# Kernel tuning notes

Hardware: AMD Instinct MI355X
Metric: run time of the kernel (lower is better)

Reference implementation:

```python
import jax, jax.numpy as jnp
import numpy as np

THETA_BASE = 10000.0

def rope(x, pos_offset=0):
    # x: (B, S, D), D even. Rotates interleaved (even, odd) dim pairs.
    B, S, D = x.shape
    pos = jnp.arange(pos_offset, pos_offset + S, dtype=jnp.float32)[:, None]  # (S,1)
    p = jnp.arange(D // 2, dtype=jnp.float32)  # p-1 in source, 0-indexed here
    theta = pos * (THETA_BASE ** (-2.0 * p / D))  # (S, D//2)
    sin_t, cos_t = jnp.sin(theta), jnp.cos(theta)
    x1, x2 = x[..., 0::2], x[..., 1::2]
    r1 = x1 * cos_t - x2 * sin_t
    r2 = x1 * sin_t + x2 * cos_t
    return jnp.stack((r1, r2), axis=-1).reshape(B, S, D)

def setup_inputs() -> dict:
    key = jax.random.key(0)
    k1, k2, k3, k4 = jax.random.split(key, 4)
    B, S, E, Dh = 4, 4096, 2048, 128
    return {
        "x": jax.random.normal(k1, (B, S, E), dtype=jnp.float32),
        "W_Q": jax.random.normal(k2, (E, Dh), dtype=jnp.float32) / np.sqrt(E),
        "W_K": jax.random.normal(k3, (E, Dh), dtype=jnp.float32) / np.sqrt(E),
        "W_V": jax.random.normal(k4, (E, Dh), dtype=jnp.float32) / np.sqrt(E),
    }

def reference(x, W_Q, W_K, W_V):
    d_h = W_Q.shape[1]
    past_len = 0  # kv_cache is None (prefill)
    Q = rope(x @ W_Q, pos_offset=past_len)  # NOTE: source ropes Q and V, not K
    K = x @ W_K
    V = rope(x @ W_V, pos_offset=past_len)
    scores = jnp.einsum('bqd,bkd->bqk', Q, K) / jnp.sqrt(jnp.float32(d_h))
    S_q, S_total = scores.shape[-2], scores.shape[-1]
    i = jnp.arange(S_q)[:, None] + past_len
    j = jnp.arange(S_total)[None, :]
    causal = j <= i  # (S_q, S_total) bool
    masked = jnp.where(causal[None, :, :], scores, jnp.float32(-jnp.inf))
    attn = jax.nn.softmax(masked, axis=-1)
    return jnp.einsum('bqk,bkd->bqd', attn, V)
```

## Files before the change

### kernel.cpp

```cpp
#include <hip/hip_runtime.h>
#include <hip/hip_bf16.h>
#include <stdint.h>

#define S_LEN 4096
#define E_DIM 2048
#define DH    128

typedef __bf16 bf16_t;
typedef bf16_t bf16x8 __attribute__((ext_vector_type(8)));
typedef float  f32x4  __attribute__((ext_vector_type(4)));

__device__ __forceinline__ unsigned short f2bf(float f) {
  union { float f; uint32_t u; } v; v.f = f;
  uint32_t u = v.u;
  uint32_t r = (u + 0x7fffu + ((u >> 16) & 1u)) >> 16;
  return (unsigned short)r;
}

__device__ __forceinline__ bf16x8 ld_bf16x8(const unsigned short* p) {
  return *(const bf16x8*)p;
}

__device__ __forceinline__ f32x4 mfma16(bf16x8 a, bf16x8 b, f32x4 c) {
  return __builtin_amdgcn_mfma_f32_16x16x32_bf16(a, b, c, 0, 0, 0);
}

__device__ __forceinline__ void gload16(const void* gsrc, void* ldst) {
  __builtin_amdgcn_global_load_lds(
      (const __attribute__((address_space(1))) uint32_t*)gsrc,
      (__attribute__((address_space(3))) uint32_t*)ldst, 16, 0, 0);
}

__global__ __launch_bounds__(256) void prep_kernel(
    const float* __restrict__ WQ, const float* __restrict__ WK,
    const float* __restrict__ WV,
    float2* __restrict__ trig, unsigned short* __restrict__ Wt)
{
  const int bx  = blockIdx.x;
  const int tid = threadIdx.x;
  if (bx < 1024) {
    const int idx = bx * 256 + tid;
    const int pos = idx >> 6, p = idx & 63;
    const float freq = powf(10000.0f, -(float)p / 64.0f);
    float sv, cv;
    sincosf((float)pos * freq, &sv, &cv);
    trig[idx] = make_float2(cv, sv);
    return;
  }
  __shared__ float lds[64][65];
  const int t   = bx - 1024;
  const int z   = t >> 6;
  const int rem = t & 63;
  const int k0  = (rem >> 1) * 64;
  const int n0  = (rem & 1) * 64;
  const float* W = (z == 0) ? WQ : ((z == 1) ? WK : WV);
  #pragma unroll
  for (int pass = 0; pass < 4; pass++) {
    const int r  = pass * 16 + (tid >> 4);
    const int c4 = (tid & 15) * 4;
    float4 v = *(const float4*)(W + (size_t)(k0 + r) * 128 + n0 + c4);
    lds[c4 + 0][r] = v.x; lds[c4 + 1][r] = v.y;
    lds[c4 + 2][r] = v.z; lds[c4 + 3][r] = v.w;
  }
  __syncthreads();
  #pragma unroll
  for (int pass = 0; pass < 4; pass++) {
    const int n  = pass * 16 + (tid >> 4);
    const int k4 = (tid & 15) * 4;
    ushort4 pk;
    pk.x = f2bf(lds[n][k4 + 0]); pk.y = f2bf(lds[n][k4 + 1]);
    pk.z = f2bf(lds[n][k4 + 2]); pk.w = f2bf(lds[n][k4 + 3]);
    *(ushort4*)(Wt + (size_t)(z * 128 + n0 + n) * E_DIM + k0 + k4) = pk;
  }
}

__global__ __launch_bounds__(256, 2) void proj_kernel(
    const float* __restrict__ x, const unsigned short* __restrict__ Wt,
    const float2* __restrict__ trig,
    unsigned short* __restrict__ Qb, unsigned short* __restrict__ Kb,
    unsigned short* __restrict__ Vt)
{
  __shared__ __align__(16) uint8_t Abuf[2][128 * 128];
  __shared__ __align__(16) uint8_t Bbuf[2][96 * 128];

  const int tid  = threadIdx.x;
  const int lane = tid & 63, w2 = tid >> 6;
  const int wr = w2 & 1, wc = w2 >> 1;
  const int col = lane & 15, kg = lane >> 4;

  const int m0 = blockIdx.x * 128;
  const int p  = blockIdx.y;

  f32x4 acc[4][3];
  #pragma unroll
  for (int i = 0; i < 4; i++)
    #pragma unroll
    for (int j = 0; j < 3; j++) acc[i][j] = (f32x4){0.f, 0.f, 0.f, 0.f};

  const int a_r = lane >> 4;
  const int a_c = (lane & 15) * 4;
  const int b_r  = lane >> 3;
  const int b_cb = (lane & 7) * 16;

  float4 a_reg[8];

  #define ALOAD(K0)                                                           \
    do {                                                                      \
      _Pragma("unroll")                                                       \
      for (int j = 0; j < 8; j++) {                                           \
        const int row = w2 * 32 + j * 4 + a_r;                                \
        a_reg[j] = *(const float4*)(x + (size_t)(m0 + row) * E_DIM + (K0) + a_c);\
      }                                                                       \
    } while (0)

  #define BSTAGE(K0, BUF)                                                     \
    do {                                                                      \
      _Pragma("unroll")                                                       \
      for (int c = 0; c < 3; c++) {                                           \
        const int seg = w2 * 3 + c;                                           \
        const int row = seg * 8 + b_r;                                        \
        const int src = b_cb ^ ((row & 7) << 4);                              \
        gload16((const char*)Wt + ((size_t)(p * 96 + row) * E_DIM + (K0)) * 2 + src,\
                &Bbuf[BUF][seg * 1024]);                                      \
      }                                                                       \
    } while (0)

  #define AWRITE(BUF)                                                         \
    do {                                                                      \
      _Pragma("unroll")                                                       \
      for (int j = 0; j < 8; j++) {                                           \
        const int row = w2 * 32 + j * 4 + a_r;                                \
        ushort4 h;                                                            \
        h.x = f2bf(a_reg[j].x); h.y = f2bf(a_reg[j].y);                       \
        h.z = f2bf(a_reg[j].z); h.w = f2bf(a_reg[j].w);                       \
        const int dst = (a_c * 2) ^ ((row & 7) << 4);                         \
        *(ushort4*)(&Abuf[BUF][row * 128 + dst]) = h;                         \
      }                                                                       \
    } while (0)

  ALOAD(0);
  BSTAGE(0, 0);
  AWRITE(0);
  __syncthreads();

  int cur = 0;
  for (int t = 0; t < 32; t++) {
    if (t < 31) {
      ALOAD((t + 1) * 64);
      BSTAGE((t + 1) * 64, cur ^ 1);
    }

    __builtin_amdgcn_s_setprio(1);
    #pragma unroll
    for (int kk = 0; kk < 2; kk++) {
      bf16x8 af[4];
      #pragma unroll
      for (int i = 0; i < 4; i++) {
        const int row = wr * 64 + i * 16 + col;
        af[i] = *(const bf16x8*)(&Abuf[cur][row * 128 +
                 ((kk * 64 + kg * 16) ^ ((row & 7) << 4))]);
      }
      #pragma unroll
      for (int ns = 0; ns < 3; ns++) {
        const int n = wc * 48 + ns * 16 + col;
        bf16x8 bf = *(const bf16x8*)(&Bbuf[cur][n * 128 +
                    ((kk * 64 + kg * 16) ^ ((n & 7) << 4))]);
        #pragma unroll
        for (int i = 0; i < 4; i++)
          acc[i][ns] = mfma16(af[i], bf, acc[i][ns]);
      }
    }
    __builtin_amdgcn_s_setprio(0);

    if (t < 31) AWRITE(cur ^ 1);
    __syncthreads();
    cur ^= 1;
  }
  #undef ALOAD
  #undef BSTAGE
  #undef AWRITE

  #pragma unroll
  for (int i = 0; i < 4; i++) {
    const int mbase = m0 + wr * 64 + i * 16 + kg * 4;
    const int spos  = mbase & 4095;
    const int bb    = mbase >> 12;
    #pragma unroll
    for (int ns = 0; ns < 3; ns++) {
      const int n = p * 96 + wc * 48 + ns * 16 + col;
      const int z = n >> 7, d = n & 127;
      f32x4 v = acc[i][ns];
      if (z == 1) {
        #pragma unroll
        for (int r = 0; r < 4; r++)
          Kb[(size_t)(mbase + r) * DH + d] = f2bf(v[r]);
      } else {
        const float sgn  = (d & 1) ? 1.0f : -1.0f;
        const int   pidx = d >> 1;
        float ov[4];
        #pragma unroll
        for (int r = 0; r < 4; r++) {
          float  pv = __shfl_xor(v[r], 1, 64);
          float2 cs = trig[(spos + r) * 64 + pidx];
          ov[r] = v[r] * cs.x + sgn * pv * cs.y;
        }
        if (z == 0) {
          #pragma unroll
          for (int r = 0; r < 4; r++)
            Qb[(size_t)(mbase + r) * DH + d] =
                f2bf(ov[r] * 0.08838834764831845f);
        } else {
          ushort4 pk;
          pk.x = f2bf(ov[0]); pk.y = f2bf(ov[1]);
          pk.z = f2bf(ov[2]); pk.w = f2bf(ov[3]);
          *(ushort4*)(Vt + ((size_t)(bb * DH + d)) * S_LEN + spos) = pk;
        }
      }
    }
  }
}

__global__ __launch_bounds__(256, 2) void flash_kernel(
    const unsigned short* __restrict__ Qb, const unsigned short* __restrict__ Kb,
    const unsigned short* __restrict__ Vt, float* __restrict__ out)
{
  __shared__ __align__(16) unsigned short Ktile[128 * 128];
  __shared__ __align__(16) unsigned short Vtile[128 * 128];
  __shared__ __align__(16) unsigned short Plds[4][16][72];

  const int bid  = blockIdx.x;
  const int half = bid >> 8, rb = bid & 255;
  const int qi   = half ? (127 - (rb >> 1)) : (rb >> 1);
  const int b    = (rb & 1) | (half << 1);
  const int q0   = qi * 32;

  const int tid = threadIdx.x;
  const int lane = tid & 63, w = tid >> 6;
  const int h   = w & 1;
  const int kvh = w >> 1;
  const int col = lane & 15, kg = lane >> 4;

  bf16x8 qf[4];
  {
    const unsigned short* qrow =
        Qb + (size_t)(b * S_LEN + q0 + h * 16 + col) * DH;
    #pragma unroll
    for (int kk = 0; kk < 4; kk++)
      qf[kk] = ld_bf16x8(qrow + kk * 32 + kg * 8);
  }

  f32x4 o[8];
  #pragma unroll
  for (int i = 0; i < 8; i++) o[i] = (f32x4){0.f, 0.f, 0.f, 0.f};
  float mrow[4] = {-1e30f, -1e30f, -1e30f, -1e30f};
  float lrow[4] = {0.f, 0.f, 0.f, 0.f};

  const char* Kbase = (const char*)(Kb + (size_t)b * S_LEN * DH);
  const char* Vbase = (const char*)(Vt + (size_t)b * DH * S_LEN);

  const int r_off = lane >> 4, colb = (lane & 15) * 16;

  for (int kv0 = 0; kv0 < q0 + 32; kv0 += 128) {
    #pragma unroll
    for (int c = 0; c < 8; c++) {
      const int row = w * 32 + c * 4 + r_off;
      const int src = colb ^ ((row & 7) << 4);
      gload16(Kbase + (size_t)(kv0 + row) * 256 + src,
              (char*)Ktile + w * 8192 + c * 1024);
    }
    #pragma unroll
    for (int c = 0; c < 8; c++) {
      const int d   = w * 32 + c * 4 + r_off;
      const int src = colb ^ ((d & 7) << 4);
      gload16(Vbase + (size_t)d * 8192 + (size_t)kv0 * 2 + src,
              (char*)Vtile + w * 8192 + c * 1024);
    }
    __syncthreads();

    f32x4 st[4];
    __builtin_amdgcn_s_setprio(1);
    #pragma unroll
    for (int kb = 0; kb < 4; kb++) {
      f32x4 sacc = (f32x4){0.f, 0.f, 0.f, 0.f};
      const int krow = kvh * 64 + kb * 16 + col;
      #pragma unroll
      for (int kk = 0; kk < 4; kk++) {
        bf16x8 kf = *(const bf16x8*)((const char*)Ktile + krow * 256 +
                                     ((kk * 64 + kg * 16) ^ ((krow & 7) << 4)));
        sacc = mfma16(qf[kk], kf, sacc);
      }
      st[kb] = sacc;
    }
    __builtin_amdgcn_s_setprio(0);

    if (kv0 + 127 > q0) {
      #pragma unroll
      for (int kb = 0; kb < 4; kb++) {
        const int key = kv0 + kvh * 64 + kb * 16 + col;
        #pragma unroll
        for (int r = 0; r < 4; r++) {
          const int q = q0 + h * 16 + kg * 4 + r;
          if (key > q) st[kb][r] = -1e30f;
        }
      }
    }

    float scale[4];
    #pragma unroll
    for (int r = 0; r < 4; r++) {
      float mx = fmaxf(fmaxf(st[0][r], st[1][r]), fmaxf(st[2][r], st[3][r]));
      #pragma unroll
      for (int off = 1; off < 16; off <<= 1)
        mx = fmaxf(mx, __shfl_xor(mx, off, 64));
      const float mnew = fmaxf(mrow[r], mx);
      scale[r] = __expf(mrow[r] - mnew);
      mrow[r] = mnew;
      float psum = 0.f;
      #pragma unroll
      for (int kb = 0; kb < 4; kb++) {
        float pexp = __expf(st[kb][r] - mnew);
        st[kb][r] = pexp;
        psum += pexp;
      }
      lrow[r] = lrow[r] * scale[r] + psum;
    }
    #pragma unroll
    for (int nt = 0; nt < 8; nt++)
      #pragma unroll
      for (int r = 0; r < 4; r++)
        o[nt][r] *= scale[r];

    #pragma unroll
    for (int kb = 0; kb < 4; kb++)
      #pragma unroll
      for (int r = 0; r < 4; r++)
        Plds[w][kg * 4 + r][kb * 16 + col] = f2bf(st[kb][r]);

    __builtin_amdgcn_s_setprio(1);
    #pragma unroll
    for (int kc = 0; kc < 2; kc++) {
      bf16x8 pa = ld_bf16x8(&Plds[w][col][kc * 32 + kg * 8]);
      #pragma unroll
      for (int nt = 0; nt < 8; nt++) {
        const int vrow = nt * 16 + col;
        bf16x8 vf = *(const bf16x8*)((const char*)Vtile + vrow * 256 +
            ((kvh * 128 + kc * 64 + kg * 16) ^ ((vrow & 7) << 4)));
        o[nt] = mfma16(pa, vf, o[nt]);
      }
    }
    __builtin_amdgcn_s_setprio(0);
    __syncthreads();
  }

  float lfull[4];
  #pragma unroll
  for (int r = 0; r < 4; r++) {
    float l = lrow[r];
    #pragma unroll
    for (int off = 1; off < 16; off <<= 1)
      l += __shfl_xor(l, off, 64);
    lfull[r] = l;
  }

  float* Olds = (float*)Ktile;
  float* Ml   = (float*)Vtile;
  #pragma unroll
  for (int nt = 0; nt < 8; nt++)
    #pragma unroll
    for (int r = 0; r < 4; r++)
      Olds[(w * 16 + kg * 4 + r) * 128 + nt * 16 + col] = o[nt][r];
  if (col == 0) {
    #pragma unroll
    for (int r = 0; r < 4; r++) {
      Ml[w * 16 + kg * 4 + r]      = mrow[r];
      Ml[64 + w * 16 + kg * 4 + r] = lfull[r];
    }
  }
  __syncthreads();
  if (w < 2) {
    #pragma unroll
    for (int r = 0; r < 4; r++) {
      const int row = kg * 4 + r;
      const float m1 = Ml[w * 16 + row],        l1 = Ml[64 + w * 16 + row];
      const float m2 = Ml[(w + 2) * 16 + row],  l2 = Ml[64 + (w + 2) * 16 + row];
      const float mf = fmaxf(m1, m2);
      const float w1 = __expf(m1 - mf), wgt2 = __expf(m2 - mf);
      const float inv = 1.0f / (l1 * w1 + l2 * wgt2);
      float* orow = out + (size_t)(b * S_LEN + q0 + w * 16 + row) * DH;
      #pragma unroll
      for (int nt = 0; nt < 8; nt++) {
        const float v1 = Olds[(w * 16 + row) * 128 + nt * 16 + col];
        const float v2 = Olds[((w + 2) * 16 + row) * 128 + nt * 16 + col];
        orow[nt * 16 + col] = (v1 * w1 + v2 * wgt2) * inv;
      }
    }
  }
}

extern "C" void kernel_launch(void* const* d_in, const int* in_sizes, int n_in,
                              void* d_out, int out_size, void* d_ws, size_t ws_size,
                              hipStream_t stream) {
  const float* x  = (const float*)d_in[0];
  const float* WQ = (const float*)d_in[1];
  const float* WK = (const float*)d_in[2];
  const float* WV = (const float*)d_in[3];
  float* out = (float*)d_out;

  char* ws = (char*)d_ws;
  float2*         trig = (float2*)(ws);
  unsigned short* Wt   = (unsigned short*)(ws + (2u << 20));
  unsigned short* Qb   = (unsigned short*)(ws + (4u << 20));
  unsigned short* Kb   = (unsigned short*)(ws + (8u << 20));
  unsigned short* Vt   = (unsigned short*)(ws + (12u << 20));

  hipLaunchKernelGGL(prep_kernel, dim3(1216), dim3(256), 0, stream,
                     WQ, WK, WV, trig, Wt);
  hipLaunchKernelGGL(proj_kernel, dim3(128, 4), dim3(256), 0, stream,
                     x, Wt, trig, Qb, Kb, Vt);
  hipLaunchKernelGGL(flash_kernel, dim3(512), dim3(256), 0, stream,
                     Qb, Kb, Vt, out);
}
```

Baseline: 136.1 us.

## Shrink flash blocks to 16 queries and load V fragments directly from global

The flash kernel now uses 128-thread blocks, each covering 16 query rows, with two waves splitting each 128-key tile, and the grid doubles to 1024 blocks. V is no longer staged in LDS; each wave loads its V fragments straight from global memory into registers. The goal is to cut LDS footprint and improve occupancy and load balance. In exchange, reuse of K/V per block drops, total global and L2 traffic roughly doubles, and the direct V loads are uncoalesced strided reads with high register pressure.

Measured after the change: 154.2 us. 1.13x slower.

```diff
diff --git a/kernel.cpp b/kernel.cpp
--- a/kernel.cpp
+++ b/kernel.cpp
@@ -220,30 +220,26 @@
   }
 }
 
-__global__ __launch_bounds__(256, 2) void flash_kernel(
+__global__ __launch_bounds__(128, 2) void flash_kernel(
     const unsigned short* __restrict__ Qb, const unsigned short* __restrict__ Kb,
     const unsigned short* __restrict__ Vt, float* __restrict__ out)
 {
   __shared__ __align__(16) unsigned short Ktile[128 * 128];
-  __shared__ __align__(16) unsigned short Vtile[128 * 128];
-  __shared__ __align__(16) unsigned short Plds[4][16][72];
+  __shared__ __align__(16) unsigned short Plds[2][16][72];
 
   const int bid  = blockIdx.x;
-  const int half = bid >> 8, rb = bid & 255;
-  const int qi   = half ? (127 - (rb >> 1)) : (rb >> 1);
+  const int half = bid >> 9, rb = bid & 511;
+  const int qi   = half ? (255 - (rb >> 1)) : (rb >> 1);
   const int b    = (rb & 1) | (half << 1);
-  const int q0   = qi * 32;
+  const int q0   = qi * 16;
 
   const int tid = threadIdx.x;
   const int lane = tid & 63, w = tid >> 6;
-  const int h   = w & 1;
-  const int kvh = w >> 1;
   const int col = lane & 15, kg = lane >> 4;
 
   bf16x8 qf[4];
   {
-    const unsigned short* qrow =
-        Qb + (size_t)(b * S_LEN + q0 + h * 16 + col) * DH;
+    const unsigned short* qrow = Qb + (size_t)(b * S_LEN + q0 + col) * DH;
     #pragma unroll
     for (int kk = 0; kk < 4; kk++)
       qf[kk] = ld_bf16x8(qrow + kk * 32 + kg * 8);
@@ -255,34 +251,37 @@
   float mrow[4] = {-1e30f, -1e30f, -1e30f, -1e30f};
   float lrow[4] = {0.f, 0.f, 0.f, 0.f};
 
-  const char* Kbase = (const char*)(Kb + (size_t)b * S_LEN * DH);
-  const char* Vbase = (const char*)(Vt + (size_t)b * DH * S_LEN);
-
-  const int r_off = lane >> 4, colb = (lane & 15) * 16;
-
-  for (int kv0 = 0; kv0 < q0 + 32; kv0 += 128) {
-    #pragma unroll
-    for (int c = 0; c < 8; c++) {
-      const int row = w * 32 + c * 4 + r_off;
-      const int src = colb ^ ((row & 7) << 4);
+  const char*           Kbase = (const char*)(Kb + (size_t)b * S_LEN * DH);
+  const unsigned short* Vbase = Vt + (size_t)b * DH * S_LEN;
+
+  const int kr  = lane >> 4;
+  const int kcb = (lane & 15) * 16;
+
+  for (int kv0 = 0; kv0 < q0 + 16; kv0 += 128) {
+    #pragma unroll
+    for (int c = 0; c < 16; c++) {
+      const int row = w * 64 + c * 4 + kr;
+      const int src = kcb ^ ((row & 7) << 4);
       gload16(Kbase + (size_t)(kv0 + row) * 256 + src,
-              (char*)Ktile + w * 8192 + c * 1024);
-    }
-    #pragma unroll
-    for (int c = 0; c < 8; c++) {
-      const int d   = w * 32 + c * 4 + r_off;
-      const int src = colb ^ ((d & 7) << 4);
-      gload16(Vbase + (size_t)d * 8192 + (size_t)kv0 * 2 + src,
-              (char*)Vtile + w * 8192 + c * 1024);
+              (char*)Ktile + (w * 64 + c * 4) * 256);
     }
     __syncthreads();
+
+    bf16x8 vreg[2][8];
+    #pragma unroll
+    for (int kc = 0; kc < 2; kc++)
+      #pragma unroll
+      for (int nt = 0; nt < 8; nt++)
+        vreg[kc][nt] = ld_bf16x8(
+            Vbase + (size_t)(nt * 16 + col) * S_LEN +
+            kv0 + w * 64 + kc * 32 + kg * 8);
 
     f32x4 st[4];
     __builtin_amdgcn_s_setprio(1);
     #pragma unroll
     for (int kb = 0; kb < 4; kb++) {
       f32x4 sacc = (f32x4){0.f, 0.f, 0.f, 0.f};
-      const int krow = kvh * 64 + kb * 16 + col;
+      const int krow = w * 64 + kb * 16 + col;
       #pragma unroll
       for (int kk = 0; kk < 4; kk++) {
         bf16x8 kf = *(const bf16x8*)((const char*)Ktile + krow * 256 +
@@ -296,10 +295,10 @@
     if (kv0 + 127 > q0) {
       #pragma unroll
       for (int kb = 0; kb < 4; kb++) {
-        const int key = kv0 + kvh * 64 + kb * 16 + col;
+        const int key = kv0 + w * 64 + kb * 16 + col;
         #pragma unroll
         for (int r = 0; r < 4; r++) {
-          const int q = q0 + h * 16 + kg * 4 + r;
+          const int q = q0 + kg * 4 + r;
           if (key > q) st[kb][r] = -1e30f;
         }
       }
@@ -341,12 +340,8 @@
     for (int kc = 0; kc < 2; kc++) {
       bf16x8 pa = ld_bf16x8(&Plds[w][col][kc * 32 + kg * 8]);
       #pragma unroll
-      for (int nt = 0; nt < 8; nt++) {
-        const int vrow = nt * 16 + col;
-        bf16x8 vf = *(const bf16x8*)((const char*)Vtile + vrow * 256 +
-            ((kvh * 128 + kc * 64 + kg * 16) ^ ((vrow & 7) << 4)));
-        o[nt] = mfma16(pa, vf, o[nt]);
-      }
+      for (int nt = 0; nt < 8; nt++)
+        o[nt] = mfma16(pa, vreg[kc][nt], o[nt]);
     }
     __builtin_amdgcn_s_setprio(0);
     __syncthreads();
@@ -363,7 +358,7 @@
   }
 
   float* Olds = (float*)Ktile;
-  float* Ml   = (float*)Vtile;
+  float* Ml   = (float*)Plds;
   #pragma unroll
   for (int nt = 0; nt < 8; nt++)
     #pragma unroll
@@ -373,24 +368,24 @@
     #pragma unroll
     for (int r = 0; r < 4; r++) {
       Ml[w * 16 + kg * 4 + r]      = mrow[r];
-      Ml[64 + w * 16 + kg * 4 + r] = lfull[r];
+      Ml[32 + w * 16 + kg * 4 + r] = lfull[r];
     }
   }
   __syncthreads();
-  if (w < 2) {
+  if (w == 0) {
     #pragma unroll
     for (int r = 0; r < 4; r++) {
       const int row = kg * 4 + r;
-      const float m1 = Ml[w * 16 + row],        l1 = Ml[64 + w * 16 + row];
-      const float m2 = Ml[(w + 2) * 16 + row],  l2 = Ml[64 + (w + 2) * 16 + row];
+      const float m1 = Ml[row],      l1 = Ml[32 + row];
+      const float m2 = Ml[16 + row], l2 = Ml[32 + 16 + row];
       const float mf = fmaxf(m1, m2);
       const float w1 = __expf(m1 - mf), wgt2 = __expf(m2 - mf);
       const float inv = 1.0f / (l1 * w1 + l2 * wgt2);
-      float* orow = out + (size_t)(b * S_LEN + q0 + w * 16 + row) * DH;
+      float* orow = out + (size_t)(b * S_LEN + q0 + row) * DH;
       #pragma unroll
       for (int nt = 0; nt < 8; nt++) {
-        const float v1 = Olds[(w * 16 + row) * 128 + nt * 16 + col];
-        const float v2 = Olds[((w + 2) * 16 + row) * 128 + nt * 16 + col];
+        const float v1 = Olds[row * 128 + nt * 16 + col];
+        const float v2 = Olds[(16 + row) * 128 + nt * 16 + col];
         orow[nt * 16 + col] = (v1 * w1 + v2 * wgt2) * inv;
       }
     }
@@ -417,6 +412,6 @@
                      WQ, WK, WV, trig, Wt);
   hipLaunchKernelGGL(proj_kernel, dim3(128, 4), dim3(256), 0, stream,
                      x, Wt, trig, Qb, Kb, Vt);
-  hipLaunchKernelGGL(flash_kernel, dim3(512), dim3(256), 0, stream,
+  hipLaunchKernelGGL(flash_kernel, dim3(1024), dim3(128), 0, stream,
                      Qb, Kb, Vt, out);
 }
```

## Prefetch next K/V tile into registers while computing current tile

Applied to the files above, without the earlier changes.

Replaces the direct global-to-LDS K/V tile loads with a register-staged software pipeline. The next tile's global loads are issued before the QK and PV MFMA work on the current tile, then written to LDS between two barriers. This aims to hide global memory latency behind compute, at the cost of 16 extra uint4 registers per thread and an extra barrier per iteration, which may lower occupancy.

Result: slower. 244.1 us (+79.4%).

```diff
diff --git a/kernel.cpp b/kernel.cpp
--- a/kernel.cpp
+++ b/kernel.cpp
@@ -260,22 +260,45 @@
 
   const int r_off = lane >> 4, colb = (lane & 15) * 16;
 
-  for (int kv0 = 0; kv0 < q0 + 32; kv0 += 128) {
-    #pragma unroll
-    for (int c = 0; c < 8; c++) {
-      const int row = w * 32 + c * 4 + r_off;
-      const int src = colb ^ ((row & 7) << 4);
-      gload16(Kbase + (size_t)(kv0 + row) * 256 + src,
-              (char*)Ktile + w * 8192 + c * 1024);
-    }
-    #pragma unroll
-    for (int c = 0; c < 8; c++) {
-      const int d   = w * 32 + c * 4 + r_off;
-      const int src = colb ^ ((d & 7) << 4);
-      gload16(Vbase + (size_t)d * 8192 + (size_t)kv0 * 2 + src,
-              (char*)Vtile + w * 8192 + c * 1024);
-    }
-    __syncthreads();
+  uint4 kreg[8], vreg[8];
+
+  #define KVLOAD(T)                                                           \
+    do {                                                                      \
+      const int kv0s = (T) * 128;                                             \
+      _Pragma("unroll")                                                       \
+      for (int c = 0; c < 8; c++) {                                           \
+        const int row = w * 32 + c * 4 + r_off;                               \
+        const int src = colb ^ ((row & 7) << 4);                              \
+        kreg[c] = *(const uint4*)(Kbase + (size_t)(kv0s + row) * 256 + src);  \
+      }                                                                       \
+      _Pragma("unroll")                                                       \
+      for (int c = 0; c < 8; c++) {                                           \
+        const int d   = w * 32 + c * 4 + r_off;                               \
+        const int src = colb ^ ((d & 7) << 4);                                \
+        vreg[c] = *(const uint4*)(Vbase + (size_t)d * 8192 +                  \
+                                  (size_t)kv0s * 2 + src);                    \
+      }                                                                       \
+    } while (0)
+
+  #define KVWRITE()                                                           \
+    do {                                                                      \
+      _Pragma("unroll")                                                       \
+      for (int c = 0; c < 8; c++)                                             \
+        *(uint4*)((char*)Ktile + w * 8192 + c * 1024 + lane * 16) = kreg[c];  \
+      _Pragma("unroll")                                                       \
+      for (int c = 0; c < 8; c++)                                             \
+        *(uint4*)((char*)Vtile + w * 8192 + c * 1024 + lane * 16) = vreg[c];  \
+    } while (0)
+
+  const int NT = (q0 + 32 + 127) >> 7;
+
+  KVLOAD(0);
+  KVWRITE();
+  __syncthreads();
+
+  for (int t = 0; t < NT; t++) {
+    const int kv0 = t * 128;
+    if (t + 1 < NT) KVLOAD(t + 1);
 
     f32x4 st[4];
     __builtin_amdgcn_s_setprio(1);
@@ -349,8 +372,15 @@
       }
     }
     __builtin_amdgcn_s_setprio(0);
-    __syncthreads();
-  }
+
+    if (t + 1 < NT) {
+      __syncthreads();
+      KVWRITE();
+      __syncthreads();
+    }
+  }
+  #undef KVLOAD
+  #undef KVWRITE
 
   float lfull[4];
   #pragma unroll
@@ -361,6 +391,8 @@
       l += __shfl_xor(l, off, 64);
     lfull[r] = l;
   }
+
+  __syncthreads();
 
   float* Olds = (float*)Ktile;
   float* Ml   = (float*)Vtile;
```
